# Kernel optimization log

Measured on AMD Instinct MI355X. Metric: run time of the kernel, lower is better.

The kernel has to match this reference:

```python
import jax, jax.numpy as jnp
import numpy as np

B, T, I = 8, 128, 196
TEXT_DIM, IMAGE_DIM, HIDDEN = 768, 1024, 512


def setup_inputs() -> dict:
    key = jax.random.key(0)
    ks = jax.random.split(key, 7)
    s = lambda d: 1.0 / np.sqrt(d)
    return {
        "text_features": jax.random.normal(ks[0], (B, T, TEXT_DIM), jnp.float32),
        "image_features": jax.random.normal(ks[1], (B, I, IMAGE_DIM), jnp.float32),
        "Wt": jax.random.normal(ks[2], (TEXT_DIM, HIDDEN), jnp.float32) * s(TEXT_DIM),
        "bt": jax.random.normal(ks[3], (HIDDEN,), jnp.float32) * s(TEXT_DIM),
        "Wi": jax.random.normal(ks[4], (IMAGE_DIM, HIDDEN), jnp.float32) * s(IMAGE_DIM),
        "bi": jax.random.normal(ks[5], (HIDDEN,), jnp.float32) * s(IMAGE_DIM),
        "wa": jax.random.normal(ks[6], (HIDDEN,), jnp.float32) * s(HIDDEN),
        "ba": jnp.zeros((1,), jnp.float32),
    }


def reference(text_features, image_features, Wt, bt, Wi, bi, wa, ba):
    # projections: [B,T,H] and [B,I,H]
    pt = jnp.einsum("btd,dh->bth", text_features, Wt) + bt
    pi = jnp.einsum("bid,dh->bih", image_features, Wi) + bi
    # additive Bahdanau scores: tanh of broadcast sum [B,T,I,H], reduced by wa
    h = jnp.tanh(pt[:, :, None, :] + pi[:, None, :, :])
    scores = jnp.einsum("btih,h->bti", h, wa) + ba[0]  # [B,T,I]
    text_attended = jnp.einsum("bti,bid->btd", jax.nn.softmax(scores, axis=-1), image_features)
    image_attended = jnp.einsum("bti,btd->bid", jax.nn.softmax(scores, axis=1), text_features)
    return text_attended, image_attended
```

## Files before the change

### kernel.cpp

```cpp
#include <hip/hip_runtime.h>
#include <math.h>

#define B 8
#define T 128
#define I_TOK 196
#define TEXT_DIM 768
#define IMAGE_DIM 1024
#define HIDDEN 512
#define EXP_SCALE 2.88539008177792681f

#if __has_builtin(__builtin_amdgcn_exp2f)
#define FAST_EXP2(x) __builtin_amdgcn_exp2f(x)
#else
#define FAST_EXP2(x) exp2f(x)
#endif
#if __has_builtin(__builtin_amdgcn_rcpf)
#define FAST_RCP(x) __builtin_amdgcn_rcpf(x)
#else
#define FAST_RCP(x) __fdividef(1.f, (x))
#endif

typedef short bf16x8 __attribute__((ext_vector_type(8)));
typedef float f32x4 __attribute__((ext_vector_type(4)));

typedef __attribute__((address_space(3))) void       as3_void;
typedef __attribute__((address_space(1))) const void as1_cvoid;

#define KT_T (TEXT_DIM / 32)
#define KT_I (IMAGE_DIM / 32)
#define MT_T (B * T / 16)
#define MT_I (B * I_TOK / 16)
#define NT   (HIDDEN / 16)

#define XT_ELEMS (MT_T * KT_T * 512)
#define XI_ELEMS (MT_I * KT_I * 512)
#define X_ELEMS  (XT_ELEMS + XI_ELEMS)
#define WT_T_ELEMS (NT * KT_T * 512)
#define W_ELEMS (WT_T_ELEMS + NT * KT_I * 512)

#define XTILES_T (MT_T * KT_T)
#define XTILES   (XTILES_T + MT_I * KT_I)
#define WTILES_T (NT * KT_T)
#define WTILES   (WTILES_T + NT * KT_I)
#define PREP_GRID ((XTILES + WTILES) / 4)

__device__ __forceinline__ unsigned short f2bf(float x) {
    unsigned int u = __float_as_uint(x);
    unsigned int r = u + 0x7FFFu + ((u >> 16) & 1u);
    return (unsigned short)(r >> 16);
}
__device__ __forceinline__ float bf2f(unsigned short h) {
    return __uint_as_float(((unsigned int)h) << 16);
}

__global__ __launch_bounds__(256) void prep_kernel(
        const float* __restrict__ text, const float* __restrict__ image,
        const float* __restrict__ Wt, const float* __restrict__ Wi,
        unsigned short* __restrict__ Xh, unsigned short* __restrict__ Xl,
        unsigned short* __restrict__ WTh, unsigned short* __restrict__ WTl)
{
    const int tid = threadIdx.x;
    const int lane = tid & 63, wv = tid >> 6;
    const int r16 = lane & 15, quad = lane >> 4;
    const int id = blockIdx.x * 4 + wv;

    float v[8];
    unsigned short* oh;
    unsigned short* ol;
    long dst;

    if (id < XTILES) {
        const float* X; int K, mt, kt;
        if (id < XTILES_T) { X = text; K = TEXT_DIM; mt = id / KT_T; kt = id % KT_T; }
        else { const int i2 = id - XTILES_T; X = image; K = IMAGE_DIM; mt = i2 / KT_I; kt = i2 % KT_I; }
        const float* src = X + (long)(mt * 16 + r16) * K + kt * 32 + quad * 8;
        const float4 a = *(const float4*)src;
        const float4 b = *(const float4*)(src + 4);
        v[0]=a.x; v[1]=a.y; v[2]=a.z; v[3]=a.w; v[4]=b.x; v[5]=b.y; v[6]=b.z; v[7]=b.w;
        oh = (id < XTILES_T) ? Xh : Xh + XT_ELEMS;
        ol = (id < XTILES_T) ? Xl : Xl + XT_ELEMS;
        const long tile = (id < XTILES_T) ? id : (long)(id - XTILES_T);
        dst = tile * 512 + lane * 8;
    } else {
        const int idw = id - XTILES;
        const float* W; int K, nt, kt;
        if (idw < WTILES_T) { W = Wt; K = TEXT_DIM; nt = idw / KT_T; kt = idw % KT_T; }
        else { const int i2 = idw - WTILES_T; W = Wi; K = IMAGE_DIM; nt = i2 / KT_I; kt = i2 % KT_I; }
        const float* src = W + (long)(kt * 32 + quad * 8) * HIDDEN + nt * 16 + r16;
        #pragma unroll
        for (int j = 0; j < 8; ++j) v[j] = src[(long)j * HIDDEN];
        oh = (idw < WTILES_T) ? WTh : WTh + WT_T_ELEMS;
        ol = (idw < WTILES_T) ? WTl : WTl + WT_T_ELEMS;
        const long tile = (idw < WTILES_T) ? idw : (long)(idw - WTILES_T);
        dst = tile * 512 + lane * 8;
    }

    uint4 hv, lv;
    unsigned int hh[8], ll[8];
    #pragma unroll
    for (int j = 0; j < 8; ++j) {
        hh[j] = f2bf(v[j]);
        ll[j] = f2bf(v[j] - bf2f((unsigned short)hh[j]));
    }
    hv.x = hh[0] | (hh[1] << 16); hv.y = hh[2] | (hh[3] << 16);
    hv.z = hh[4] | (hh[5] << 16); hv.w = hh[6] | (hh[7] << 16);
    lv.x = ll[0] | (ll[1] << 16); lv.y = ll[2] | (ll[3] << 16);
    lv.z = ll[4] | (ll[5] << 16); lv.w = ll[6] | (ll[7] << 16);
    *(uint4*)(oh + dst) = hv;
    *(uint4*)(ol + dst) = lv;
}

#define GT2_BLOCKS (16 * 8)
#define GI2_BLOCKS (25 * 8)
#define GEMM_GRID (GT2_BLOCKS + GI2_BLOCKS)

__global__ __launch_bounds__(512, 4) void mfma_proj_kernel(
        const unsigned short* __restrict__ Xh, const unsigned short* __restrict__ Xl,
        const unsigned short* __restrict__ WTh, const unsigned short* __restrict__ WTl,
        const float* __restrict__ bt, const float* __restrict__ bi,
        float* __restrict__ pt, float* __restrict__ pi)
{
    __shared__ __align__(16) unsigned short lds[4][16][512];

    const int tid = threadIdx.x;
    const int lane = tid & 63, wv = tid >> 6;
    const int r16 = lane & 15, quad = lane >> 4;
    const int wr = wv >> 2, wc = wv & 3;

    const int bid0 = blockIdx.x;
    int bid;
    if (bid0 < GT2_BLOCKS) bid = (bid0 & 7) * 16 + (bid0 >> 3);
    else { const int d = bid0 - GT2_BLOCKS; bid = GT2_BLOCKS + (d & 7) * 25 + (d >> 3); }

    const unsigned short *xh, *xl, *wh, *wl; const float* bias; float* Y;
    int ktiles, mt0, n8;
    if (bid < GT2_BLOCKS) {
        xh = Xh; xl = Xl; wh = WTh; wl = WTl; bias = bt; Y = pt; ktiles = KT_T;
        mt0 = (bid >> 3) * 4; n8 = bid & 7;
    } else {
        const int ib = bid - GT2_BLOCKS;
        xh = Xh + XT_ELEMS; xl = Xl + XT_ELEMS;
        wh = WTh + WT_T_ELEMS; wl = WTl + WT_T_ELEMS;
        bias = bi; Y = pi; ktiles = KT_I;
        const int mg = ib >> 3;
        mt0 = (mg == 24) ? (MT_I - 4) : mg * 4;
        n8 = ib & 7;
    }
    const int nt0 = n8 * 4;

    const unsigned short* ssrc[2];
    #pragma unroll
    for (int q = 0; q < 2; ++q) {
        const int t = wv * 2 + q;
        const int g = t >> 2;
        const int i = t & 3;
        const unsigned short* base = (g == 0) ? xh : (g == 1) ? xl : (g == 2) ? wh : wl;
        const long row = (g < 2) ? (long)(mt0 + i) : (long)(nt0 + i);
        ssrc[q] = base + row * ktiles * 512 + lane * 8;
    }

#define STAGE(buf, kt) do {                                                    \
        _Pragma("unroll")                                                      \
        for (int q_ = 0; q_ < 2; ++q_) {                                       \
            __builtin_amdgcn_global_load_lds(                                  \
                (as1_cvoid*)(ssrc[q_] + (long)(kt) * 512),                     \
                (as3_void*)&lds[buf][wv * 2 + q_][0], 16, 0, 0);               \
        } } while (0)

    f32x4 a0 = {0,0,0,0}, a1 = {0,0,0,0};

    STAGE(0, 0);
    STAGE(1, 1);
    STAGE(2, 2);
    STAGE(3, 3);

    for (int s = 0; s < ktiles; ++s) {
        if (s + 3 < ktiles)      asm volatile("s_waitcnt vmcnt(6)" ::: "memory");
        else if (s + 2 < ktiles) asm volatile("s_waitcnt vmcnt(4)" ::: "memory");
        else if (s + 1 < ktiles) asm volatile("s_waitcnt vmcnt(2)" ::: "memory");
        else                     asm volatile("s_waitcnt vmcnt(0)" ::: "memory");
        __builtin_amdgcn_s_barrier();

        const int cur = s & 3;
        const int fo = lane * 8;
        const bf16x8 Ah0 = *(const bf16x8*)&lds[cur][wr * 2 + 0][fo];
        const bf16x8 Ah1 = *(const bf16x8*)&lds[cur][wr * 2 + 1][fo];
        const bf16x8 Al0 = *(const bf16x8*)&lds[cur][4 + wr * 2 + 0][fo];
        const bf16x8 Al1 = *(const bf16x8*)&lds[cur][4 + wr * 2 + 1][fo];
        const bf16x8 Bh  = *(const bf16x8*)&lds[cur][8 + wc][fo];
        const bf16x8 Bl  = *(const bf16x8*)&lds[cur][12 + wc][fo];

        a0 = __builtin_amdgcn_mfma_f32_16x16x32_bf16(Ah0, Bh, a0, 0, 0, 0);
        a1 = __builtin_amdgcn_mfma_f32_16x16x32_bf16(Ah1, Bh, a1, 0, 0, 0);
        a0 = __builtin_amdgcn_mfma_f32_16x16x32_bf16(Ah0, Bl, a0, 0, 0, 0);
        a1 = __builtin_amdgcn_mfma_f32_16x16x32_bf16(Ah1, Bl, a1, 0, 0, 0);
        a0 = __builtin_amdgcn_mfma_f32_16x16x32_bf16(Al0, Bh, a0, 0, 0, 0);
        a1 = __builtin_amdgcn_mfma_f32_16x16x32_bf16(Al1, Bh, a1, 0, 0, 0);

        __builtin_amdgcn_s_barrier();
        if (s + 4 < ktiles) STAGE(cur, s + 4);
    }
#undef STAGE

    const int row00 = (mt0 + wr * 2) * 16 + quad * 4;
    const int col0  = (nt0 + wc) * 16 + r16;
    const float bv = bias[col0];
    #pragma unroll
    for (int r = 0; r < 4; ++r) {
        Y[(long)(row00 + r)      * HIDDEN + col0] = FAST_EXP2((a0[r] + bv) * EXP_SCALE);
        Y[(long)(row00 + 16 + r) * HIDDEN + col0] = FAST_EXP2((a1[r] + bv) * EXP_SCALE);
    }
}

__global__ __launch_bounds__(256, 6) void scores_kernel(const float* __restrict__ pt,
        const float* __restrict__ pi, const float* __restrict__ wa,
        const float* __restrict__ ba, float* __restrict__ scores)
{
    const int blk = blockIdx.x;
    const int chunk = blk & 3;
    const int bt0 = (blk >> 2) * 2;
    const int b = bt0 >> 7;
    const int tid = threadIdx.x;
    const int lane = tid & 63, wave = tid >> 6;

    const float* ptrow = pt + (long)bt0 * HIDDEN + lane * 8;
    const float4 pA0 = *(const float4*)ptrow;
    const float4 pB0 = *(const float4*)(ptrow + 4);
    const float4 pA1 = *(const float4*)(ptrow + HIDDEN);
    const float4 pB1 = *(const float4*)(ptrow + HIDDEN + 4);
    float4 wA = *(const float4*)(wa + lane * 8);
    float4 wB = *(const float4*)(wa + lane * 8 + 4);

    float S = wA.x + wA.y + wA.z + wA.w + wB.x + wB.y + wB.z + wB.w;
    #pragma unroll
    for (int off = 32; off; off >>= 1) S += __shfl_down(S, off);
    const float base = S + ba[0];

    wA.x *= -2.f; wA.y *= -2.f; wA.z *= -2.f; wA.w *= -2.f;
    wB.x *= -2.f; wB.y *= -2.f; wB.z *= -2.f; wB.w *= -2.f;

    const float* pib = pi + (long)b * I_TOK * HIDDEN + lane * 8;
    const int i0 = chunk * 49 + wave;
    const int iend = chunk * 49 + 49;

    float4 ca = *(const float4*)(pib + (long)i0 * HIDDEN);
    float4 cb = *(const float4*)(pib + (long)i0 * HIDDEN + 4);

    for (int i = i0; i < iend; i += 4) {
        const int inx = (i + 4 < iend) ? (i + 4) : i;
        const float4 na = *(const float4*)(pib + (long)inx * HIDDEN);
        const float4 nb = *(const float4*)(pib + (long)inx * HIDDEN + 4);

        float acc0 = 0.f;
        acc0 = fmaf(wA.x, FAST_RCP(fmaf(pA0.x, ca.x, 1.f)), acc0);
        acc0 = fmaf(wA.y, FAST_RCP(fmaf(pA0.y, ca.y, 1.f)), acc0);
        acc0 = fmaf(wA.z, FAST_RCP(fmaf(pA0.z, ca.z, 1.f)), acc0);
        acc0 = fmaf(wA.w, FAST_RCP(fmaf(pA0.w, ca.w, 1.f)), acc0);
        acc0 = fmaf(wB.x, FAST_RCP(fmaf(pB0.x, cb.x, 1.f)), acc0);
        acc0 = fmaf(wB.y, FAST_RCP(fmaf(pB0.y, cb.y, 1.f)), acc0);
        acc0 = fmaf(wB.z, FAST_RCP(fmaf(pB0.z, cb.z, 1.f)), acc0);
        acc0 = fmaf(wB.w, FAST_RCP(fmaf(pB0.w, cb.w, 1.f)), acc0);

        float acc1 = 0.f;
        acc1 = fmaf(wA.x, FAST_RCP(fmaf(pA1.x, ca.x, 1.f)), acc1);
        acc1 = fmaf(wA.y, FAST_RCP(fmaf(pA1.y, ca.y, 1.f)), acc1);
        acc1 = fmaf(wA.z, FAST_RCP(fmaf(pA1.z, ca.z, 1.f)), acc1);
        acc1 = fmaf(wA.w, FAST_RCP(fmaf(pA1.w, ca.w, 1.f)), acc1);
        acc1 = fmaf(wB.x, FAST_RCP(fmaf(pB1.x, cb.x, 1.f)), acc1);
        acc1 = fmaf(wB.y, FAST_RCP(fmaf(pB1.y, cb.y, 1.f)), acc1);
        acc1 = fmaf(wB.z, FAST_RCP(fmaf(pB1.z, cb.z, 1.f)), acc1);
        acc1 = fmaf(wB.w, FAST_RCP(fmaf(pB1.w, cb.w, 1.f)), acc1);

        #pragma unroll
        for (int off = 32; off; off >>= 1) {
            acc0 += __shfl_down(acc0, off);
            acc1 += __shfl_down(acc1, off);
        }
        if (lane == 0) {
            scores[(long)bt0 * I_TOK + i]       = base + acc0;
            scores[(long)(bt0 + 1) * I_TOK + i] = base + acc1;
        }
        ca = na; cb = nb;
    }
}

#define ATT_P1_BLOCKS 512
#define ATT_P2_BLOCKS (B * 28)
#define ATT_GRID (ATT_P1_BLOCKS + ATT_P2_BLOCKS)

__global__ __launch_bounds__(256) void att_kernel(const float* __restrict__ scores,
        const float* __restrict__ image, const float* __restrict__ text,
        float* __restrict__ out_text, float* __restrict__ out_img)
{
    const int tid = threadIdx.x, lane = tid & 63, wave = tid >> 6;

    if (blockIdx.x < ATT_P1_BLOCKS) {
        const int bid = blockIdx.x;
        const int csplit = bid & 3;
        const int grp = bid >> 2;
        const int b = grp >> 4;
        const int t0 = (grp & 15) * 8;

        __shared__ float ps[I_TOK][8];
        #pragma unroll
        for (int rr = 0; rr < 2; ++rr) {
            const int tsub = wave + rr * 4;
            const float* srow = scores + ((long)(b * T + t0 + tsub)) * I_TOK;
            const float s0 = srow[lane];
            const float s1 = srow[lane + 64];
            const float s2 = srow[lane + 128];
            const float s3 = (lane < 4) ? srow[lane + 192] : -INFINITY;
            float m = fmaxf(fmaxf(s0, s1), fmaxf(s2, s3));
            #pragma unroll
            for (int off = 32; off; off >>= 1) m = fmaxf(m, __shfl_xor(m, off));
            const float e0 = __expf(s0 - m);
            const float e1 = __expf(s1 - m);
            const float e2 = __expf(s2 - m);
            const float e3 = (lane < 4) ? __expf(s3 - m) : 0.f;
            float sum = e0 + e1 + e2 + e3;
            #pragma unroll
            for (int off = 32; off; off >>= 1) sum += __shfl_xor(sum, off);
            const float inv = __fdividef(1.0f, sum);
            ps[lane][tsub] = e0 * inv;
            ps[lane + 64][tsub] = e1 * inv;
            ps[lane + 128][tsub] = e2 * inv;
            if (lane < 4) ps[lane + 192][tsub] = e3 * inv;
        }
        __syncthreads();

        const float* img = image + (long)b * I_TOK * IMAGE_DIM + csplit * 256 + tid;
        float a0 = 0.f, a1 = 0.f, a2 = 0.f, a3 = 0.f;
        float a4 = 0.f, a5 = 0.f, a6 = 0.f, a7 = 0.f;

        float vA0 = img[0 * IMAGE_DIM];
        float vA1 = img[1 * IMAGE_DIM];
        float vA2 = img[2 * IMAGE_DIM];
        float vA3 = img[3 * IMAGE_DIM];
        float vB0 = img[4 * IMAGE_DIM];
        float vB1 = img[5 * IMAGE_DIM];
        float vB2 = img[6 * IMAGE_DIM];
        float vB3 = img[7 * IMAGE_DIM];
        float4 pL0 = *(const float4*)&ps[0][0]; float4 pH0 = *(const float4*)&ps[0][4];
        float4 pL1 = *(const float4*)&ps[1][0]; float4 pH1 = *(const float4*)&ps[1][4];
        float4 pL2 = *(const float4*)&ps[2][0]; float4 pH2 = *(const float4*)&ps[2][4];
        float4 pL3 = *(const float4*)&ps[3][0]; float4 pH3 = *(const float4*)&ps[3][4];

        for (int g = 0; g < 49; ++g) {
            const int ib2 = ((g + 2 < 49) ? (g + 2) : 48) * 4;
            const float t0_ = img[(long)(ib2 + 0) * IMAGE_DIM];
            const float t1_ = img[(long)(ib2 + 1) * IMAGE_DIM];
            const float t2_ = img[(long)(ib2 + 2) * IMAGE_DIM];
            const float t3_ = img[(long)(ib2 + 3) * IMAGE_DIM];
            const int ibn = ((g + 1 < 49) ? (g + 1) : 48) * 4;
            const float4 nL0 = *(const float4*)&ps[ibn + 0][0]; const float4 nH0 = *(const float4*)&ps[ibn + 0][4];
            const float4 nL1 = *(const float4*)&ps[ibn + 1][0]; const float4 nH1 = *(const float4*)&ps[ibn + 1][4];
            const float4 nL2 = *(const float4*)&ps[ibn + 2][0]; const float4 nH2 = *(const float4*)&ps[ibn + 2][4];
            const float4 nL3 = *(const float4*)&ps[ibn + 3][0]; const float4 nH3 = *(const float4*)&ps[ibn + 3][4];

#define ATT_ROW(vr, pl, ph)                                                   \
            a0 = fmaf(pl.x, vr, a0); a1 = fmaf(pl.y, vr, a1);                 \
            a2 = fmaf(pl.z, vr, a2); a3 = fmaf(pl.w, vr, a3);                 \
            a4 = fmaf(ph.x, vr, a4); a5 = fmaf(ph.y, vr, a5);                 \
            a6 = fmaf(ph.z, vr, a6); a7 = fmaf(ph.w, vr, a7);
            ATT_ROW(vA0, pL0, pH0)
            ATT_ROW(vA1, pL1, pH1)
            ATT_ROW(vA2, pL2, pH2)
            ATT_ROW(vA3, pL3, pH3)
#undef ATT_ROW
            vA0 = vB0; vA1 = vB1; vA2 = vB2; vA3 = vB3;
            vB0 = t0_; vB1 = t1_; vB2 = t2_; vB3 = t3_;
            pL0 = nL0; pH0 = nH0; pL1 = nL1; pH1 = nH1;
            pL2 = nL2; pH2 = nH2; pL3 = nL3; pH3 = nH3;
        }
        float* o = out_text + ((long)(b * T + t0)) * IMAGE_DIM + csplit * 256 + tid;
        o[0 * IMAGE_DIM] = a0;
        o[1 * IMAGE_DIM] = a1;
        o[2 * IMAGE_DIM] = a2;
        o[3 * IMAGE_DIM] = a3;
        o[4 * IMAGE_DIM] = a4;
        o[5 * IMAGE_DIM] = a5;
        o[6 * IMAGE_DIM] = a6;
        o[7 * IMAGE_DIM] = a7;
    } else {
        const int bid = blockIdx.x - ATT_P1_BLOCKS;
        const int b = bid / 28;
        const int i0 = (bid % 28) * 7;

        __shared__ float qs[T][8];
        for (int cc = wave; cc < 7; cc += 4) {
            const float* sc = scores + (long)b * T * I_TOK + (i0 + cc);
            const float s0 = sc[(long)lane * I_TOK];
            const float s1 = sc[(long)(lane + 64) * I_TOK];
            float m = fmaxf(s0, s1);
            #pragma unroll
            for (int off = 32; off; off >>= 1) m = fmaxf(m, __shfl_xor(m, off));
            const float e0 = __expf(s0 - m);
            const float e1 = __expf(s1 - m);
            float sum = e0 + e1;
            #pragma unroll
            for (int off = 32; off; off >>= 1) sum += __shfl_xor(sum, off);
            const float inv = __fdividef(1.0f, sum);
            qs[lane][cc] = e0 * inv;
            qs[lane + 64][cc] = e1 * inv;
        }
        __syncthreads();

        const float* txt2 = text + (long)b * T * TEXT_DIM + tid * 2;
        const float* txt1 = text + (long)b * T * TEXT_DIM + 512 + tid;
        float ax[7], ay[7], az[7];
        #pragma unroll
        for (int r = 0; r < 7; ++r) { ax[r] = 0.f; ay[r] = 0.f; az[r] = 0.f; }

        float2 uA0 = *(const float2*)(txt2 + 0 * TEXT_DIM);
        float2 uA1 = *(const float2*)(txt2 + 1 * TEXT_DIM);
        float  zA0 = txt1[0 * TEXT_DIM];
        float  zA1 = txt1[1 * TEXT_DIM];
        float2 uB0 = *(const float2*)(txt2 + 2 * TEXT_DIM);
        float2 uB1 = *(const float2*)(txt2 + 3 * TEXT_DIM);
        float  zB0 = txt1[2 * TEXT_DIM];
        float  zB1 = txt1[3 * TEXT_DIM];
        float4 qa0 = *(const float4*)&qs[0][0]; float4 qb0 = *(const float4*)&qs[0][4];
        float4 qa1 = *(const float4*)&qs[1][0]; float4 qb1 = *(const float4*)&qs[1][4];

        for (int g = 0; g < 64; ++g) {
            const int tb2 = ((g + 2 < 64) ? (g + 2) : 63) * 2;
            const float2 tu0 = *(const float2*)(txt2 + (long)(tb2 + 0) * TEXT_DIM);
            const float2 tu1 = *(const float2*)(txt2 + (long)(tb2 + 1) * TEXT_DIM);
            const float  tz0 = txt1[(long)(tb2 + 0) * TEXT_DIM];
            const float  tz1 = txt1[(long)(tb2 + 1) * TEXT_DIM];
            const int tbn = ((g + 1 < 64) ? (g + 1) : 63) * 2;
            const float4 na0 = *(const float4*)&qs[tbn + 0][0];
            const float4 nb0 = *(const float4*)&qs[tbn + 0][4];
            const float4 na1 = *(const float4*)&qs[tbn + 1][0];
            const float4 nb1 = *(const float4*)&qs[tbn + 1][4];

            ax[0] = fmaf(qa0.x, uA0.x, ax[0]); ay[0] = fmaf(qa0.x, uA0.y, ay[0]); az[0] = fmaf(qa0.x, zA0, az[0]);
            ax[1] = fmaf(qa0.y, uA0.x, ax[1]); ay[1] = fmaf(qa0.y, uA0.y, ay[1]); az[1] = fmaf(qa0.y, zA0, az[1]);
            ax[2] = fmaf(qa0.z, uA0.x, ax[2]); ay[2] = fmaf(qa0.z, uA0.y, ay[2]); az[2] = fmaf(qa0.z, zA0, az[2]);
            ax[3] = fmaf(qa0.w, uA0.x, ax[3]); ay[3] = fmaf(qa0.w, uA0.y, ay[3]); az[3] = fmaf(qa0.w, zA0, az[3]);
            ax[4] = fmaf(qb0.x, uA0.x, ax[4]); ay[4] = fmaf(qb0.x, uA0.y, ay[4]); az[4] = fmaf(qb0.x, zA0, az[4]);
            ax[5] = fmaf(qb0.y, uA0.x, ax[5]); ay[5] = fmaf(qb0.y, uA0.y, ay[5]); az[5] = fmaf(qb0.y, zA0, az[5]);
            ax[6] = fmaf(qb0.z, uA0.x, ax[6]); ay[6] = fmaf(qb0.z, uA0.y, ay[6]); az[6] = fmaf(qb0.z, zA0, az[6]);
            ax[0] = fmaf(qa1.x, uA1.x, ax[0]); ay[0] = fmaf(qa1.x, uA1.y, ay[0]); az[0] = fmaf(qa1.x, zA1, az[0]);
            ax[1] = fmaf(qa1.y, uA1.x, ax[1]); ay[1] = fmaf(qa1.y, uA1.y, ay[1]); az[1] = fmaf(qa1.y, zA1, az[1]);
            ax[2] = fmaf(qa1.z, uA1.x, ax[2]); ay[2] = fmaf(qa1.z, uA1.y, ay[2]); az[2] = fmaf(qa1.z, zA1, az[2]);
            ax[3] = fmaf(qa1.w, uA1.x, ax[3]); ay[3] = fmaf(qa1.w, uA1.y, ay[3]); az[3] = fmaf(qa1.w, zA1, az[3]);
            ax[4] = fmaf(qb1.x, uA1.x, ax[4]); ay[4] = fmaf(qb1.x, uA1.y, ay[4]); az[4] = fmaf(qb1.x, zA1, az[4]);
            ax[5] = fmaf(qb1.y, uA1.x, ax[5]); ay[5] = fmaf(qb1.y, uA1.y, ay[5]); az[5] = fmaf(qb1.y, zA1, az[5]);
            ax[6] = fmaf(qb1.z, uA1.x, ax[6]); ay[6] = fmaf(qb1.z, uA1.y, ay[6]); az[6] = fmaf(qb1.z, zA1, az[6]);

            uA0 = uB0; uA1 = uB1; zA0 = zB0; zA1 = zB1;
            uB0 = tu0; uB1 = tu1; zB0 = tz0; zB1 = tz1;
            qa0 = na0; qb0 = nb0; qa1 = na1; qb1 = nb1;
        }
        float* o = out_img + ((long)b * I_TOK + i0) * TEXT_DIM;
        #pragma unroll
        for (int r = 0; r < 7; ++r) {
            float2 w;
            w.x = ax[r]; w.y = ay[r];
            *(float2*)(o + (long)r * TEXT_DIM + tid * 2) = w;
            o[(long)r * TEXT_DIM + 512 + tid] = az[r];
        }
    }
}

extern "C" void kernel_launch(void* const* d_in, const int* in_sizes, int n_in,
                              void* d_out, int out_size, void* d_ws, size_t ws_size,
                              hipStream_t stream) {
    const float* text  = (const float*)d_in[0];
    const float* image = (const float*)d_in[1];
    const float* Wt    = (const float*)d_in[2];
    const float* bt    = (const float*)d_in[3];
    const float* Wi    = (const float*)d_in[4];
    const float* bi    = (const float*)d_in[5];
    const float* wa    = (const float*)d_in[6];
    const float* ba    = (const float*)d_in[7];

    float* pt = (float*)d_ws;
    float* pi = pt + (long)B * T * HIDDEN;
    float* sc = pi + (long)B * I_TOK * HIDDEN;
    unsigned short* Xh  = (unsigned short*)(sc + (long)B * T * I_TOK);
    unsigned short* Xl  = Xh + X_ELEMS;
    unsigned short* WTh = Xl + X_ELEMS;
    unsigned short* WTl = WTh + W_ELEMS;

    float* out_text = (float*)d_out;
    float* out_img  = out_text + (long)B * T * IMAGE_DIM;

    prep_kernel<<<PREP_GRID, 256, 0, stream>>>(text, image, Wt, Wi, Xh, Xl, WTh, WTl);
    mfma_proj_kernel<<<GEMM_GRID, 512, 0, stream>>>(Xh, Xl, WTh, WTl, bt, bi, pt, pi);
    scores_kernel<<<2 * B * T, 256, 0, stream>>>(pt, pi, wa, ba, sc);
    att_kernel<<<ATT_GRID, 256, 0, stream>>>(sc, image, text, out_text, out_img);
}
```

Measured before the change: 130.6 us.

## Transpose image projection output and remap scores kernel to lane-per-image-token

The projection kernel now writes the exponentiated image projection transposed (hidden-major, rows contiguous) so the scores kernel can give each lane one image token and loop over the hidden dimension. pt and wa are read as wave-uniform values, which removes the per-token cross-lane shuffle reductions. The -2 scaling is applied once at the end. The grid drops to one block per pair of text rows, with 4 waves covering 196 tokens (15 idle lanes per wave), which lowers parallelism. Strided column loads from the transposed buffer may also be less coalesced.

New measurement: 147.4 us. +12.9%, slower.

```diff
diff --git a/kernel.cpp b/kernel.cpp
--- a/kernel.cpp
+++ b/kernel.cpp
@@ -7,6 +7,7 @@
 #define TEXT_DIM 768
 #define IMAGE_DIM 1024
 #define HIDDEN 512
+#define NROWI (B * I_TOK)
 #define EXP_SCALE 2.88539008177792681f
 
 #if __has_builtin(__builtin_amdgcn_exp2f)
@@ -118,7 +119,7 @@
         const unsigned short* __restrict__ Xh, const unsigned short* __restrict__ Xl,
         const unsigned short* __restrict__ WTh, const unsigned short* __restrict__ WTl,
         const float* __restrict__ bt, const float* __restrict__ bi,
-        float* __restrict__ pt, float* __restrict__ pi)
+        float* __restrict__ pt, float* __restrict__ piT)
 {
     __shared__ __align__(16) unsigned short lds[4][16][512];
 
@@ -134,14 +135,15 @@
 
     const unsigned short *xh, *xl, *wh, *wl; const float* bias; float* Y;
     int ktiles, mt0, n8;
-    if (bid < GT2_BLOCKS) {
+    const bool is_text = (bid < GT2_BLOCKS);
+    if (is_text) {
         xh = Xh; xl = Xl; wh = WTh; wl = WTl; bias = bt; Y = pt; ktiles = KT_T;
         mt0 = (bid >> 3) * 4; n8 = bid & 7;
     } else {
         const int ib = bid - GT2_BLOCKS;
         xh = Xh + XT_ELEMS; xl = Xl + XT_ELEMS;
         wh = WTh + WT_T_ELEMS; wl = WTl + WT_T_ELEMS;
-        bias = bi; Y = pi; ktiles = KT_I;
+        bias = bi; Y = piT; ktiles = KT_I;
         const int mg = ib >> 3;
         mt0 = (mg == 24) ? (MT_I - 4) : mg * 4;
         n8 = ib & 7;
@@ -205,82 +207,78 @@
     const int row00 = (mt0 + wr * 2) * 16 + quad * 4;
     const int col0  = (nt0 + wc) * 16 + r16;
     const float bv = bias[col0];
-    #pragma unroll
-    for (int r = 0; r < 4; ++r) {
-        Y[(long)(row00 + r)      * HIDDEN + col0] = FAST_EXP2((a0[r] + bv) * EXP_SCALE);
-        Y[(long)(row00 + 16 + r) * HIDDEN + col0] = FAST_EXP2((a1[r] + bv) * EXP_SCALE);
-    }
-}
-
-__global__ __launch_bounds__(256, 6) void scores_kernel(const float* __restrict__ pt,
-        const float* __restrict__ pi, const float* __restrict__ wa,
+    if (is_text) {
+        #pragma unroll
+        for (int r = 0; r < 4; ++r) {
+            Y[(long)(row00 + r)      * HIDDEN + col0] = FAST_EXP2((a0[r] + bv) * EXP_SCALE);
+            Y[(long)(row00 + 16 + r) * HIDDEN + col0] = FAST_EXP2((a1[r] + bv) * EXP_SCALE);
+        }
+    } else {
+        float4 v0, v1;
+        v0.x = FAST_EXP2((a0[0] + bv) * EXP_SCALE);
+        v0.y = FAST_EXP2((a0[1] + bv) * EXP_SCALE);
+        v0.z = FAST_EXP2((a0[2] + bv) * EXP_SCALE);
+        v0.w = FAST_EXP2((a0[3] + bv) * EXP_SCALE);
+        v1.x = FAST_EXP2((a1[0] + bv) * EXP_SCALE);
+        v1.y = FAST_EXP2((a1[1] + bv) * EXP_SCALE);
+        v1.z = FAST_EXP2((a1[2] + bv) * EXP_SCALE);
+        v1.w = FAST_EXP2((a1[3] + bv) * EXP_SCALE);
+        *(float4*)(Y + (long)col0 * NROWI + row00)      = v0;
+        *(float4*)(Y + (long)col0 * NROWI + row00 + 16) = v1;
+    }
+}
+
+__global__ __launch_bounds__(256) void scores_kernel(const float* __restrict__ pt,
+        const float* __restrict__ piT, const float* __restrict__ wa,
         const float* __restrict__ ba, float* __restrict__ scores)
 {
     const int blk = blockIdx.x;
-    const int chunk = blk & 3;
-    const int bt0 = (blk >> 2) * 2;
+    const int bt0 = blk * 2;
     const int b = bt0 >> 7;
     const int tid = threadIdx.x;
-    const int lane = tid & 63, wave = tid >> 6;
-
-    const float* ptrow = pt + (long)bt0 * HIDDEN + lane * 8;
-    const float4 pA0 = *(const float4*)ptrow;
-    const float4 pB0 = *(const float4*)(ptrow + 4);
-    const float4 pA1 = *(const float4*)(ptrow + HIDDEN);
-    const float4 pB1 = *(const float4*)(ptrow + HIDDEN + 4);
-    float4 wA = *(const float4*)(wa + lane * 8);
-    float4 wB = *(const float4*)(wa + lane * 8 + 4);
-
-    float S = wA.x + wA.y + wA.z + wA.w + wB.x + wB.y + wB.z + wB.w;
+    const int lane = tid & 63, wv = tid >> 6;
+    const int il = wv * 49 + ((lane < 49) ? lane : 48);
+
+    float base;
+    {
+        const float4 wA = *(const float4*)(wa + lane * 8);
+        const float4 wB = *(const float4*)(wa + lane * 8 + 4);
+        float S = wA.x + wA.y + wA.z + wA.w + wB.x + wB.y + wB.z + wB.w;
+        #pragma unroll
+        for (int off = 32; off; off >>= 1) S += __shfl_down(S, off);
+        S = __shfl(S, 0);
+        base = S + ba[0];
+    }
+
+    const float* __restrict__ pt0 = pt + (long)bt0 * HIDDEN;
+    const float* __restrict__ pt1 = pt0 + HIDDEN;
+    const float* __restrict__ col = piT + (long)b * I_TOK + il;
+
+    float q0a = 0.f, q0b = 0.f, q1a = 0.f, q1b = 0.f;
+    float e[8], en[8];
     #pragma unroll
-    for (int off = 32; off; off >>= 1) S += __shfl_down(S, off);
-    const float base = S + ba[0];
-
-    wA.x *= -2.f; wA.y *= -2.f; wA.z *= -2.f; wA.w *= -2.f;
-    wB.x *= -2.f; wB.y *= -2.f; wB.z *= -2.f; wB.w *= -2.f;
-
-    const float* pib = pi + (long)b * I_TOK * HIDDEN + lane * 8;
-    const int i0 = chunk * 49 + wave;
-    const int iend = chunk * 49 + 49;
-
-    float4 ca = *(const float4*)(pib + (long)i0 * HIDDEN);
-    float4 cb = *(const float4*)(pib + (long)i0 * HIDDEN + 4);
-
-    for (int i = i0; i < iend; i += 4) {
-        const int inx = (i + 4 < iend) ? (i + 4) : i;
-        const float4 na = *(const float4*)(pib + (long)inx * HIDDEN);
-        const float4 nb = *(const float4*)(pib + (long)inx * HIDDEN + 4);
-
-        float acc0 = 0.f;
-        acc0 = fmaf(wA.x, FAST_RCP(fmaf(pA0.x, ca.x, 1.f)), acc0);
-        acc0 = fmaf(wA.y, FAST_RCP(fmaf(pA0.y, ca.y, 1.f)), acc0);
-        acc0 = fmaf(wA.z, FAST_RCP(fmaf(pA0.z, ca.z, 1.f)), acc0);
-        acc0 = fmaf(wA.w, FAST_RCP(fmaf(pA0.w, ca.w, 1.f)), acc0);
-        acc0 = fmaf(wB.x, FAST_RCP(fmaf(pB0.x, cb.x, 1.f)), acc0);
-        acc0 = fmaf(wB.y, FAST_RCP(fmaf(pB0.y, cb.y, 1.f)), acc0);
-        acc0 = fmaf(wB.z, FAST_RCP(fmaf(pB0.z, cb.z, 1.f)), acc0);
-        acc0 = fmaf(wB.w, FAST_RCP(fmaf(pB0.w, cb.w, 1.f)), acc0);
-
-        float acc1 = 0.f;
-        acc1 = fmaf(wA.x, FAST_RCP(fmaf(pA1.x, ca.x, 1.f)), acc1);
-        acc1 = fmaf(wA.y, FAST_RCP(fmaf(pA1.y, ca.y, 1.f)), acc1);
-        acc1 = fmaf(wA.z, FAST_RCP(fmaf(pA1.z, ca.z, 1.f)), acc1);
-        acc1 = fmaf(wA.w, FAST_RCP(fmaf(pA1.w, ca.w, 1.f)), acc1);
-        acc1 = fmaf(wB.x, FAST_RCP(fmaf(pB1.x, cb.x, 1.f)), acc1);
-        acc1 = fmaf(wB.y, FAST_RCP(fmaf(pB1.y, cb.y, 1.f)), acc1);
-        acc1 = fmaf(wB.z, FAST_RCP(fmaf(pB1.z, cb.z, 1.f)), acc1);
-        acc1 = fmaf(wB.w, FAST_RCP(fmaf(pB1.w, cb.w, 1.f)), acc1);
-
-        #pragma unroll
-        for (int off = 32; off; off >>= 1) {
-            acc0 += __shfl_down(acc0, off);
-            acc1 += __shfl_down(acc1, off);
-        }
-        if (lane == 0) {
-            scores[(long)bt0 * I_TOK + i]       = base + acc0;
-            scores[(long)(bt0 + 1) * I_TOK + i] = base + acc1;
-        }
-        ca = na; cb = nb;
+    for (int j = 0; j < 8; ++j) e[j] = col[(long)j * NROWI];
+
+    #pragma unroll 1
+    for (int h = 0; h < HIDDEN; h += 8) {
+        const int hn = (h + 8 < HIDDEN) ? (h + 8) : h;
+        #pragma unroll
+        for (int j = 0; j < 8; ++j) en[j] = col[(long)(hn + j) * NROWI];
+
+        #pragma unroll
+        for (int j = 0; j < 8; j += 2) {
+            q0a = fmaf(wa[h + j],     FAST_RCP(fmaf(pt0[h + j],     e[j],     1.f)), q0a);
+            q1a = fmaf(wa[h + j],     FAST_RCP(fmaf(pt1[h + j],     e[j],     1.f)), q1a);
+            q0b = fmaf(wa[h + j + 1], FAST_RCP(fmaf(pt0[h + j + 1], e[j + 1], 1.f)), q0b);
+            q1b = fmaf(wa[h + j + 1], FAST_RCP(fmaf(pt1[h + j + 1], e[j + 1], 1.f)), q1b);
+        }
+        #pragma unroll
+        for (int j = 0; j < 8; ++j) e[j] = en[j];
+    }
+
+    if (lane < 49) {
+        scores[(long)bt0 * I_TOK + il]       = fmaf(-2.f, q0a + q0b, base);
+        scores[(long)(bt0 + 1) * I_TOK + il] = fmaf(-2.f, q1a + q1b, base);
     }
 }
 
@@ -476,9 +474,9 @@
     const float* wa    = (const float*)d_in[6];
     const float* ba    = (const float*)d_in[7];
 
-    float* pt = (float*)d_ws;
-    float* pi = pt + (long)B * T * HIDDEN;
-    float* sc = pi + (long)B * I_TOK * HIDDEN;
+    float* pt  = (float*)d_ws;
+    float* piT = pt + (long)B * T * HIDDEN;
+    float* sc  = piT + (long)HIDDEN * NROWI;
     unsigned short* Xh  = (unsigned short*)(sc + (long)B * T * I_TOK);
     unsigned short* Xl  = Xh + X_ELEMS;
     unsigned short* WTh = Xl + X_ELEMS;
@@ -488,7 +486,7 @@
     float* out_img  = out_text + (long)B * T * IMAGE_DIM;
 
     prep_kernel<<<PREP_GRID, 256, 0, stream>>>(text, image, Wt, Wi, Xh, Xl, WTh, WTl);
-    mfma_proj_kernel<<<GEMM_GRID, 512, 0, stream>>>(Xh, Xl, WTh, WTl, bt, bi, pt, pi);
-    scores_kernel<<<2 * B * T, 256, 0, stream>>>(pt, pi, wa, ba, sc);
+    mfma_proj_kernel<<<GEMM_GRID, 512, 0, stream>>>(Xh, Xl, WTh, WTl, bt, bi, pt, piT);
+    scores_kernel<<<B * T / 2, 256, 0, stream>>>(pt, piT, wa, ba, sc);
     att_kernel<<<ATT_GRID, 256, 0, stream>>>(sc, image, text, out_text, out_img);
 }
```
